# Kernel tuning notes

Hardware: AMD Instinct MI355X
Metric: run time of the kernel (lower is better)

The kernel has to match this reference:

```python
import jax, jax.numpy as jnp
import numpy as np

B, L, H, NH = 4, 2048, 1024, 8
DK = H // NH   # head_k_dim = 128
DV = H // NH   # head_v_dim = 128
CONV_K, FIR_S, FIR_L = 4, 3, 31
CMAX = 0.2
EPS = 1e-5
CHUNK = 32


def _l2norm(x):
    return x * jax.lax.rsqrt(jnp.sum(x * x, -1, keepdims=True) + 1e-6)


def _rms(x, w):
    return x * jax.lax.rsqrt(jnp.mean(x * x, -1, keepdims=True) + EPS) * w


def _causal_conv(x, w):
    # x: [b, l, d], w: [d, K] depthwise causal FIR (ShortConvolution)
    K = w.shape[1]
    l = x.shape[1]
    xp = jnp.pad(x, ((0, 0), (K - 1, 0), (0, 0)))
    return sum(xp[:, i:i + l, :] * w[:, i][None, None, :] for i in range(K))


def _fir(x, w):
    # x: [b, l, h, d], w: [h, d, K] per-head depthwise causal FIR
    K = w.shape[-1]
    l = x.shape[1]
    xp = jnp.pad(x, ((0, 0), (K - 1, 0), (0, 0), (0, 0)))
    return sum(xp[:, i:i + l] * w[:, :, i][None, None] for i in range(K))


def _delta_rule_chunkwise(q, k, v, beta, chunk=CHUNK):
    # q,k: [b,h,L,dk]; v: [b,h,L,dv]; beta: [b,h,L]; L % chunk == 0
    b, h, Ln, dk = q.shape
    dv = v.shape[-1]
    n = Ln // chunk
    q = _l2norm(q)
    k = _l2norm(k)
    v = v * beta[..., None]
    kb = k * beta[..., None]
    rs = lambda t: t.reshape(b, h, n, chunk, t.shape[-1])
    qc, kc, vc, kbc = rs(q), rs(k), rs(v), rs(kb)
    mask_incl = jnp.triu(jnp.ones((chunk, chunk), dtype=bool), 0)
    mask_strict = jnp.triu(jnp.ones((chunk, chunk), dtype=bool), 1)
    # UT / WY transform: sequential Gaussian-elimination over chunk rows
    attn = jnp.where(mask_incl, 0.0, -(kbc @ jnp.swapaxes(kc, -1, -2)))
    for i in range(1, chunk):
        row = attn[..., i, :]                                   # [b,h,n,c]
        upd = jnp.einsum('bhnj,bhnjk->bhnk', row, attn[..., :i])  # [b,h,n,i]
        attn = attn.at[..., i, :i].add(upd)
    attn = attn + jnp.eye(chunk, dtype=attn.dtype)
    u = attn @ vc    # [b,h,n,c,dv]
    w = attn @ kbc   # [b,h,n,c,dk]
    # sequential scan over chunks carrying state S [b,h,dk,dv]
    mv = lambda t: jnp.moveaxis(t, 2, 0)  # [n,b,h,c,d]
    def step(S, xs):
        q_i, k_i, u_i, w_i = xs
        attn_local = jnp.where(mask_strict, 0.0, q_i @ jnp.swapaxes(k_i, -1, -2))
        u_new = u_i - w_i @ S
        o_i = q_i @ S + attn_local @ u_new
        S = S + jnp.swapaxes(k_i, -1, -2) @ u_new
        return S, o_i
    S0 = jnp.zeros((b, h, dk, dv), dtype=q.dtype)
    S, o = jax.lax.scan(step, S0, (mv(qc), mv(kc), mv(u), mv(w)))
    o = jnp.moveaxis(o, 0, 2).reshape(b, h, Ln, dv)
    return o, S


def _forward(hidden_states, Wq, Wk, Wv, Wb, conv_q_w, conv_k_w, conv_v_w,
             fir_short_w, fir_long_w, floor_W, floor_b, fus_W1, fus_b1,
             fus_W2, fus_b2, norm_pf_w, norm_o_w, Wo):
    b, l, _ = hidden_states.shape
    hs = hidden_states
    q_lin = jax.nn.silu(_causal_conv(hs @ Wq, conv_q_w))
    k_lin = jax.nn.silu(_causal_conv(hs @ Wk, conv_k_w))
    v_lin = jax.nn.silu(_causal_conv(hs @ Wv, conv_v_w))
    q = q_lin.reshape(b, l, NH, DK)
    k = k_lin.reshape(b, l, NH, DK)
    v_direct = v_lin.reshape(b, l, NH, DV)
    beta = jax.nn.sigmoid(hs @ Wb)  # [b,l,h]
    delta_out_t, _ = _delta_rule_chunkwise(
        jnp.transpose(q, (0, 2, 1, 3)), jnp.transpose(k, (0, 2, 1, 3)),
        jnp.transpose(v_direct, (0, 2, 1, 3)), jnp.transpose(beta, (0, 2, 1)))
    delta_out = jnp.transpose(delta_out_t, (0, 2, 1, 3))  # [b,l,h,dv]
    local_short = _fir(v_direct, fir_short_w)
    local_long = _fir(v_direct, fir_long_w)
    floor = jax.nn.sigmoid(hs @ floor_W + floor_b) * CMAX  # [b,l,h]
    fus = jax.nn.gelu(hs @ fus_W1 + fus_b1, approximate=False) @ fus_W2 + fus_b2
    fus = fus.reshape(b, l, NH, 4)
    p_value = jax.nn.sigmoid(fus[..., 3]) * (1.0 - floor)  # context share >= floor
    ctx = jax.nn.softmax(fus[..., :3], axis=-1) * (1.0 - p_value)[..., None]
    o = (ctx[..., 0, None] * local_short + ctx[..., 1, None] * local_long
         + ctx[..., 2, None] * delta_out + p_value[..., None] * v_direct)
    o = _rms(o, norm_pf_w)
    o = _rms(o, norm_o_w)
    return o.reshape(b, l, NH * DV) @ Wo


def setup_inputs() -> dict:
    key = jax.random.key(0)
    ks = jax.random.split(key, 16)
    n = lambda k, shape, s=0.02: jax.random.normal(k, shape, jnp.float32) * s
    fus_b2 = jnp.zeros((NH * 4,), jnp.float32).at[3::4].set(4.0)
    return {
        'hidden_states': jax.random.normal(ks[0], (B, L, H), jnp.float32),
        'Wq': n(ks[1], (H, H)), 'Wk': n(ks[2], (H, H)), 'Wv': n(ks[3], (H, H)),
        'Wb': n(ks[4], (H, NH)),
        'conv_q_w': n(ks[5], (H, CONV_K), 0.2),
        'conv_k_w': n(ks[6], (H, CONV_K), 0.2),
        'conv_v_w': n(ks[7], (H, CONV_K), 0.2),
        'fir_short_w': n(ks[8], (NH, DV, FIR_S), 0.2),
        'fir_long_w': n(ks[9], (NH, DV, FIR_L), 0.2),
        'floor_W': n(ks[10], (H, NH)),
        'floor_b': jnp.full((NH,), float(np.log(CMAX / (1 - CMAX))), jnp.float32),
        'fus_W1': n(ks[11], (H, 2 * H)), 'fus_b1': jnp.zeros((2 * H,), jnp.float32),
        'fus_W2': n(ks[12], (2 * H, NH * 4)), 'fus_b2': fus_b2,
        'norm_pf_w': jnp.ones((DV,), jnp.float32),
        'norm_o_w': jnp.ones((DV,), jnp.float32),
        'Wo': n(ks[13], (H, H)),
    }


def reference(hidden_states, Wq, Wk, Wv, Wb, conv_q_w, conv_k_w, conv_v_w,
              fir_short_w, fir_long_w, floor_W, floor_b, fus_W1, fus_b1,
              fus_W2, fus_b2, norm_pf_w, norm_o_w, Wo):
    return _forward(hidden_states, Wq, Wk, Wv, Wb, conv_q_w, conv_k_w, conv_v_w,
                    fir_short_w, fir_long_w, floor_W, floor_b, fus_W1, fus_b1,
                    fus_W2, fus_b2, norm_pf_w, norm_o_w, Wo)
```

## Files before the change

### kernel.cpp

```cpp
#include <hip/hip_runtime.h>
#include <hip/hip_bf16.h>
#include <cstdint>
#include <cstddef>

#define DEVI static __device__ __forceinline__

typedef __attribute__((ext_vector_type(4))) float f32x4;
typedef __attribute__((ext_vector_type(8))) short s16x8;
typedef unsigned short u16;
typedef unsigned int u32;

DEVI float bf2f(u16 u){ u32 x = ((u32)u) << 16; float f; __builtin_memcpy(&f, &x, 4); return f; }
DEVI u16 f2bf(float f){ u32 x; __builtin_memcpy(&x, &f, 4); u32 r = x + 0x7fffu + ((x >> 16) & 1u); return (u16)(r >> 16); }
DEVI float sigm(float x){ return 1.0f / (1.0f + expf(-x)); }
DEVI f32x4 mfma16(s16x8 a, s16x8 b, f32x4 c){ return __builtin_amdgcn_mfma_f32_16x16x32_bf16(a, b, c, 0, 0, 0); }
DEVI s16x8 pack8(float4 a, float4 b){
  s16x8 v;
  v[0]=(short)f2bf(a.x); v[1]=(short)f2bf(a.y); v[2]=(short)f2bf(a.z); v[3]=(short)f2bf(a.w);
  v[4]=(short)f2bf(b.x); v[5]=(short)f2bf(b.y); v[6]=(short)f2bf(b.z); v[7]=(short)f2bf(b.w);
  return v;
}
DEVI u32 pkbf(float lo, float hi){
  u32 d; asm("v_cvt_pk_bf16_f32 %0, %1, %2" : "=v"(d) : "v"(lo), "v"(hi));
  return d;
}
DEVI s16x8 ld_tr(const u16* p){
  short4 a = *(const short4*)p;
  short4 b = *(const short4*)(p + 4);
  s16x8 v; v[0]=a.x; v[1]=a.y; v[2]=a.z; v[3]=a.w; v[4]=b.x; v[5]=b.y; v[6]=b.z; v[7]=b.w;
  return v;
}

#define GLL16(gp, lp) __builtin_amdgcn_global_load_lds( \
    (const __attribute__((address_space(1))) void*)(gp), \
    (__attribute__((address_space(3))) void*)(lp), 16, 0, 0)

__global__ __launch_bounds__(256) void cvt_bf16_k(const float* __restrict__ src, u16* __restrict__ dst, int n4){
  int i = blockIdx.x * 256 + threadIdx.x;
  if (i < n4){
    float4 v = ((const float4*)src)[i];
    ushort4 o; o.x = f2bf(v.x); o.y = f2bf(v.y); o.z = f2bf(v.z); o.w = f2bf(v.w);
    ((ushort4*)dst)[i] = o;
  }
}

__global__ __launch_bounds__(256) void transpose_bf16_k(const float* __restrict__ src, u16* __restrict__ dst, int K, int N){
  __shared__ float tile[32][33];
  const int n0 = blockIdx.x * 32, k0 = blockIdx.y * 32;
  const int t = threadIdx.x, cc = t & 31, rb = t >> 5;
  #pragma unroll
  for (int it = 0; it < 4; ++it){ int rr = rb + it*8; tile[rr][cc] = src[(size_t)(k0+rr)*N + n0 + cc]; }
  __syncthreads();
  #pragma unroll
  for (int it = 0; it < 4; ++it){ int rr = rb + it*8; dst[(size_t)(n0+rr)*K + k0 + cc] = f2bf(tile[cc][rr]); }
}

__global__ __launch_bounds__(64) void w2pack_k(const float* __restrict__ W2, u16* __restrict__ w2p){
  const int kt = blockIdx.x, nt = blockIdx.y;
  const int lane = threadIdx.x, g = lane >> 4, r = lane & 15;
  float v[8];
  #pragma unroll
  for (int i=0;i<8;++i) v[i] = W2[(size_t)(kt*32 + g*8 + i)*32 + nt*16 + r];
  *(s16x8*)(w2p + (((size_t)kt*2 + nt)*64 + lane)*8) = pack8(make_float4(v[0],v[1],v[2],v[3]),
                                                             make_float4(v[4],v[5],v[6],v[7]));
}

__global__ __launch_bounds__(64) void wbpack_k(const float* __restrict__ Wb, const float* __restrict__ Wfl,
                                              u16* __restrict__ wbp){
  const int kt = blockIdx.x;
  const int lane = threadIdx.x, g = lane >> 4, r = lane & 15;
  float v[8];
  #pragma unroll
  for (int i=0;i<8;++i){
    const int k = kt*32 + g*8 + i;
    v[i] = (r < 8) ? Wb[(size_t)k*8 + r] : Wfl[(size_t)k*8 + (r-8)];
  }
  *(s16x8*)(wbp + ((size_t)kt*64 + lane)*8) = pack8(make_float4(v[0],v[1],v[2],v[3]),
                                                    make_float4(v[4],v[5],v[6],v[7]));
}

template<int EPI>
__global__ __launch_bounds__(256, 2) void gemm_bt(
    const u16* __restrict__ A, const u16* __restrict__ Bt, void* __restrict__ Cout,
    const float* __restrict__ bias, int M, int N, int K)
{
  __shared__ __align__(16) u16 As[128*64];
  __shared__ __align__(16) u16 Bs[128*64];
  const int t = threadIdx.x;
  const int lane = t & 63, w = t >> 6;
  const int wr = w >> 1, wc = w & 1;
  const int g = lane >> 4, r16 = lane & 15;
  const int nwg = gridDim.x * gridDim.y;
  const int bid = blockIdx.x + blockIdx.y * gridDim.x;
  const int swz = (bid & 7) * (nwg >> 3) + (bid >> 3);
  const int m0 = (swz / gridDim.x) * 128, n0 = (swz % gridDim.x) * 128;
  f32x4 acc[4][4];
  #pragma unroll
  for (int i=0;i<4;++i){ f32x4 z = {0,0,0,0}; acc[i][0]=z; acc[i][1]=z; acc[i][2]=z; acc[i][3]=z; }
  const int NK = K / 64;
  const int slot_l = w*64 + lane;
  for (int kt = 0; kt < NK; ++kt){
    __syncthreads();
    #pragma unroll
    for (int j=0;j<4;++j){
      const int sl = j*256 + slot_l;
      const int row = sl >> 3, ch = sl & 7;
      const int chs = ch ^ (row & 7);
      GLL16(A  + (size_t)(m0+row)*K + kt*64 + chs*8, As + (size_t)(j*256 + w*64)*8);
      GLL16(Bt + (size_t)(n0+row)*K + kt*64 + chs*8, Bs + (size_t)(j*256 + w*64)*8);
    }
    __syncthreads();
    #pragma unroll
    for (int kh = 0; kh < 2; ++kh){
      s16x8 af[4], bf_[4];
      #pragma unroll
      for (int i=0;i<4;++i){
        const int arow = wr*64 + i*16 + r16;
        af[i]  = *(const s16x8*)(As + (size_t)arow*64 + (((4*kh+g) ^ (arow&7)))*8);
        const int brow = wc*64 + i*16 + r16;
        bf_[i] = *(const s16x8*)(Bs + (size_t)brow*64 + (((4*kh+g) ^ (brow&7)))*8);
      }
      #pragma unroll
      for (int mi=0;mi<4;++mi)
        #pragma unroll
        for (int ni=0;ni<4;++ni)
          acc[mi][ni] = mfma16(af[mi], bf_[ni], acc[mi][ni]);
    }
  }
  #pragma unroll
  for (int mi=0;mi<4;++mi)
    #pragma unroll
    for (int ni=0;ni<4;++ni){
      const int col = n0 + wc*64 + ni*16 + r16;
      #pragma unroll
      for (int i=0;i<4;++i){
        const int row = m0 + wr*64 + mi*16 + g*4 + i;
        float v = acc[mi][ni][i];
        if (EPI == 0){
          ((u16*)Cout)[(size_t)row*N + col] = f2bf(v);
        } else if (EPI == 1){
          float x = v + bias[col];
          x = 0.5f * x * (1.0f + erff(x * 0.70710678118f));
          ((u16*)Cout)[(size_t)row*N + col] = f2bf(x);
        } else if (EPI == 2){
          ((float*)Cout)[(size_t)row*N + col] = v;
        } else {
          ((u16*)Cout)[(size_t)(col >> 10)*8388608 + (size_t)row*1024 + (col & 1023)] = f2bf(v);
        }
      }
    }
}

__global__ __launch_bounds__(64) void beta_floor_k(
    const u16* __restrict__ hsb, const u16* __restrict__ wbp, const float* __restrict__ flb,
    float* __restrict__ beta, float* __restrict__ flo)
{
  const int m0 = blockIdx.x * 16;
  const int lane = threadIdx.x, g = lane >> 4, r = lane & 15;
  f32x4 acc0 = {0,0,0,0}, acc1 = {0,0,0,0};
  #pragma unroll 4
  for (int kt = 0; kt < 32; kt += 2){
    s16x8 a0 = *(const s16x8*)(hsb + (size_t)(m0+r)*1024 + kt*32 + g*8);
    s16x8 b0 = *(const s16x8*)(wbp + ((size_t)kt*64 + lane)*8);
    s16x8 a1 = *(const s16x8*)(hsb + (size_t)(m0+r)*1024 + (kt+1)*32 + g*8);
    s16x8 b1 = *(const s16x8*)(wbp + ((size_t)(kt+1)*64 + lane)*8);
    acc0 = mfma16(a0, b0, acc0);
    acc1 = mfma16(a1, b1, acc1);
  }
  const float fb = (r >= 8) ? flb[r-8] : 0.f;
  #pragma unroll
  for (int i=0;i<4;++i){
    const int row = m0 + g*4 + i;
    const float v = acc0[i] + acc1[i];
    if (r < 8) beta[(size_t)row*8 + r] = sigm(v);
    else       flo [(size_t)row*8 + (r-8)] = 0.2f * sigm(v + fb);
  }
}

__global__ __launch_bounds__(256) void conv_silu_k(
    const u16* __restrict__ qraw, const u16* __restrict__ kraw, const u16* __restrict__ vraw,
    const float* __restrict__ cwq, const float* __restrict__ cwk, const float* __restrict__ cwv,
    u16* __restrict__ vdir, u16* __restrict__ qn, u16* __restrict__ kn)
{
  const int blk = blockIdx.x;
  const int b = blk >> 7, lt = blk & 127;
  const int l0 = lt * 16;
  const int t = threadIdx.x, c0 = t * 4;
  float wq[16], wk[16], wv[16];
  #pragma unroll
  for (int cc=0; cc<4; ++cc){
    float4 a = *(const float4*)(cwq + (size_t)(c0+cc)*4);
    wq[cc*4+0]=a.x; wq[cc*4+1]=a.y; wq[cc*4+2]=a.z; wq[cc*4+3]=a.w;
    float4 bq = *(const float4*)(cwk + (size_t)(c0+cc)*4);
    wk[cc*4+0]=bq.x; wk[cc*4+1]=bq.y; wk[cc*4+2]=bq.z; wk[cc*4+3]=bq.w;
    float4 c = *(const float4*)(cwv + (size_t)(c0+cc)*4);
    wv[cc*4+0]=c.x; wv[cc*4+1]=c.y; wv[cc*4+2]=c.z; wv[cc*4+3]=c.w;
  }
  float hq[3][4], hk[3][4], hv[3][4];
  #pragma unroll
  for (int i=0;i<3;++i){
    const int ls = l0 - 3 + i;
    if (ls >= 0){
      const size_t base = ((size_t)(b << 11) + ls)*1024 + c0;
      union{ ushort4 v; u16 s[4]; } xq, xk, xv;
      xq.v = *(const ushort4*)(qraw + base);
      xk.v = *(const ushort4*)(kraw + base);
      xv.v = *(const ushort4*)(vraw + base);
      #pragma unroll
      for (int cc=0;cc<4;++cc){ hq[i][cc]=bf2f(xq.s[cc]); hk[i][cc]=bf2f(xk.s[cc]); hv[i][cc]=bf2f(xv.s[cc]); }
    } else {
      #pragma unroll
      for (int cc=0;cc<4;++cc){ hq[i][cc]=0.f; hk[i][cc]=0.f; hv[i][cc]=0.f; }
    }
  }
  float cq[4], ck4[4], cv4[4], nq[4], nk[4], nv[4];
  {
    const size_t base = ((size_t)(b << 11) + l0)*1024 + c0;
    union{ ushort4 v; u16 s[4]; } xq, xk, xv;
    xq.v = *(const ushort4*)(qraw + base);
    xk.v = *(const ushort4*)(kraw + base);
    xv.v = *(const ushort4*)(vraw + base);
    #pragma unroll
    for (int cc=0;cc<4;++cc){ cq[cc]=bf2f(xq.s[cc]); ck4[cc]=bf2f(xk.s[cc]); cv4[cc]=bf2f(xv.s[cc]); }
  }
  const int head = c0 >> 7, d0 = c0 & 127;
  for (int rr = 0; rr < 16; ++rr){
    const int l = l0 + rr;
    if (rr < 15){
      const size_t base = ((size_t)(b << 11) + l + 1)*1024 + c0;
      union{ ushort4 v; u16 s[4]; } xq, xk, xv;
      xq.v = *(const ushort4*)(qraw + base);
      xk.v = *(const ushort4*)(kraw + base);
      xv.v = *(const ushort4*)(vraw + base);
      #pragma unroll
      for (int cc=0;cc<4;++cc){ nq[cc]=bf2f(xq.s[cc]); nk[cc]=bf2f(xk.s[cc]); nv[cc]=bf2f(xv.s[cc]); }
    }
    float qa[4], ka[4], va[4];
    #pragma unroll
    for (int cc=0; cc<4; ++cc){
      qa[cc] = hq[0][cc]*wq[cc*4+0] + hq[1][cc]*wq[cc*4+1] + hq[2][cc]*wq[cc*4+2] + cq[cc]*wq[cc*4+3];
      ka[cc] = hk[0][cc]*wk[cc*4+0] + hk[1][cc]*wk[cc*4+1] + hk[2][cc]*wk[cc*4+2] + ck4[cc]*wk[cc*4+3];
      va[cc] = hv[0][cc]*wv[cc*4+0] + hv[1][cc]*wv[cc*4+1] + hv[2][cc]*wv[cc*4+2] + cv4[cc]*wv[cc*4+3];
    }
    #pragma unroll
    for (int cc=0; cc<4; ++cc){
      qa[cc] = qa[cc]*sigm(qa[cc]); ka[cc] = ka[cc]*sigm(ka[cc]); va[cc] = va[cc]*sigm(va[cc]);
    }
    const int grow = (b << 11) + l;
    ushort4 ov; ov.x=f2bf(va[0]); ov.y=f2bf(va[1]); ov.z=f2bf(va[2]); ov.w=f2bf(va[3]);
    *(ushort4*)(vdir + (size_t)grow*1024 + c0) = ov;
    float ssq = 0.f, ssk = 0.f;
    #pragma unroll
    for (int cc=0; cc<4; ++cc){ ssq += qa[cc]*qa[cc]; ssk += ka[cc]*ka[cc]; }
    #pragma unroll
    for (int m=1; m<32; m<<=1){ ssq += __shfl_xor(ssq, m, 64); ssk += __shfl_xor(ssk, m, 64); }
    const float rq = rsqrtf(ssq + 1e-6f), rk = rsqrtf(ssk + 1e-6f);
    const size_t ob = (((size_t)(b*8 + head))*2048 + l)*128 + d0;
    ushort4 oq, ok;
    oq.x=f2bf(qa[0]*rq); oq.y=f2bf(qa[1]*rq); oq.z=f2bf(qa[2]*rq); oq.w=f2bf(qa[3]*rq);
    ok.x=f2bf(ka[0]*rk); ok.y=f2bf(ka[1]*rk); ok.z=f2bf(ka[2]*rk); ok.w=f2bf(ka[3]*rk);
    *(ushort4*)(qn + ob) = oq;
    *(ushort4*)(kn + ob) = ok;
    #pragma unroll
    for (int cc=0; cc<4; ++cc){
      hq[0][cc]=hq[1][cc]; hq[1][cc]=hq[2][cc]; hq[2][cc]=cq[cc];  cq[cc]=nq[cc];
      hk[0][cc]=hk[1][cc]; hk[1][cc]=hk[2][cc]; hk[2][cc]=ck4[cc]; ck4[cc]=nk[cc];
      hv[0][cc]=hv[1][cc]; hv[1][cc]=hv[2][cc]; hv[2][cc]=cv4[cc]; cv4[cc]=nv[cc];
    }
  }
}

__global__ __launch_bounds__(64) void fus2_k(
    const u16* __restrict__ A, const u16* __restrict__ w2p, const float* __restrict__ b2,
    float* __restrict__ out)
{
  const int m0 = blockIdx.x * 16;
  const int lane = threadIdx.x, g = lane >> 4, r = lane & 15;
  f32x4 acc[2][2];
  #pragma unroll
  for (int nt=0;nt<2;++nt){ f32x4 z = {0,0,0,0}; acc[nt][0]=z; acc[nt][1]=z; }
  #pragma unroll 4
  for (int kt = 0; kt < 64; ++kt){
    s16x8 af = *(const s16x8*)(A + (size_t)(m0+r)*2048 + kt*32 + g*8);
    s16x8 b0 = *(const s16x8*)(w2p + (((size_t)kt*2 + 0)*64 + lane)*8);
    s16x8 b1 = *(const s16x8*)(w2p + (((size_t)kt*2 + 1)*64 + lane)*8);
    acc[0][kt&1] = mfma16(af, b0, acc[0][kt&1]);
    acc[1][kt&1] = mfma16(af, b1, acc[1][kt&1]);
  }
  #pragma unroll
  for (int nt=0;nt<2;++nt){
    const float bb = b2[nt*16 + r];
    #pragma unroll
    for (int i=0;i<4;++i)
      out[(size_t)(m0 + g*4 + i)*32 + nt*16 + r] = acc[nt][0][i] + acc[nt][1][i] + bb;
  }
}

__global__ __launch_bounds__(256, 2) void ut_k(
    const u16* __restrict__ qn, const u16* __restrict__ kn,
    const u16* __restrict__ vdir, const float* __restrict__ beta,
    u16* __restrict__ alocp, u16* __restrict__ updk,
    u16* __restrict__ wpk, u16* __restrict__ knpk)
{
  __shared__ __align__(16) char smem[39680];
  u16*  k_s = (u16*)smem;
  float* Tm = (float*)smem;
  float* Gm = (float*)(smem + 8192);
  float* al = (float*)(smem + 12416);
  float* wl = (float*)(smem + 8192);
  u16*  knT = (u16*)(smem + 17024);
  u16*  vbT = (u16*)(smem + 28288);
  float* bet = (float*)(smem + 39552);

  const int blk = blockIdx.x;
  const int ic = blk & 63, bh = blk >> 6;
  const int b = bh >> 3, h = bh & 7;
  const int l0 = ic * 32;
  const int t = threadIdx.x;
  const int lane = t & 63, w = t >> 6;
  const int g = lane >> 4, r = lane & 15;
  const int mt = w >> 1, nt_g = w & 1;

  const size_t gqk = ((size_t)bh*2048 + l0)*128;

  {
    const int row = t >> 3, sseg = t & 7;
    #pragma unroll
    for (int ss=0; ss<2; ++ss){
      const int s = sseg + ss*8;
      int4 kv = *(const int4*)(kn + gqk + (size_t)row*128 + s*8);
      *(int4*)((char*)k_s + row*256 + ((s ^ (row&7))*16)) = kv;
    }
  }
  {
    const int rp = t & 15, cs = t >> 4;
    const int r0 = 2*rp, r1 = 2*rp + 1;
    union { s16x8 v; u16 u[8]; } k0, k1, v0, v1;
    k0.v = *(const s16x8*)(kn + gqk + (size_t)r0*128 + cs*8);
    k1.v = *(const s16x8*)(kn + gqk + (size_t)r1*128 + cs*8);
    v0.v = *(const s16x8*)(vdir + ((size_t)b*2048 + l0 + r0)*1024 + h*128 + cs*8);
    v1.v = *(const s16x8*)(vdir + ((size_t)b*2048 + l0 + r1)*1024 + h*128 + cs*8);
    const float be0 = beta[((size_t)b*2048 + l0 + r0)*8 + h];
    const float be1 = beta[((size_t)b*2048 + l0 + r1)*8 + h];
    if (t < 32) bet[t] = beta[((size_t)b*2048 + l0 + t)*8 + h];
    #pragma unroll
    for (int i=0;i<8;++i){
      const int d = cs*8 + i;
      *(u32*)(knT + (size_t)d*44 + r0) = (u32)k0.u[i] | ((u32)k1.u[i] << 16);
      u32 lo = f2bf(bf2f(v0.u[i]) * be0);
      u32 hi = f2bf(bf2f(v1.u[i]) * be1);
      *(u32*)(vbT + (size_t)d*44 + r0) = lo | (hi << 16);
    }
  }
  __syncthreads();

  {
    f32x4 gacc = {0,0,0,0}, aacc = {0,0,0,0};
    #pragma unroll
    for (int kt=0; kt<4; ++kt){
      s16x8 afk = *(const s16x8*)(kn + gqk + (size_t)(mt*16+r)*128 + kt*32 + g*8);
      s16x8 afq = *(const s16x8*)(qn + gqk + (size_t)(mt*16+r)*128 + kt*32 + g*8);
      const int brow = nt_g*16 + r;
      s16x8 bfrag = *(const s16x8*)((const char*)k_s + brow*256 + (((kt*4+g) ^ (brow&7))*16));
      gacc = mfma16(afk, bfrag, gacc);
      aacc = mfma16(afq, bfrag, aacc);
    }
    #pragma unroll
    for (int i=0;i<4;++i){
      const int rr = mt*16 + g*4 + i, cc = nt_g*16 + r;
      Gm[rr*33 + cc] = gacc[i];
      al[rr*36 + cc] = (cc <= rr) ? aacc[i] : 0.f;
    }
  }
  __syncthreads();

  if (w == 0){
    const int kk = lane & 15, grp = (lane >> 4) & 1, b0 = grp*16;
    float tc[16];
    #pragma unroll
    for (int j=0;j<16;++j)
      tc[j] = (j > kk) ? (-bet[b0+j] * Gm[(b0+j)*33 + b0+kk]) : 0.f;
    #pragma unroll
    for (int i=1;i<16;++i){
      float upd = 0.f;
      #pragma unroll
      for (int j=0;j<i;++j) upd += __shfl(tc[i], (lane & 48) + j, 64) * tc[j];
      if (kk < i) tc[i] += upd;
    }
    if (lane < 32){
      #pragma unroll
      for (int j=0;j<16;++j) Tm[(b0+j)*36 + b0+kk] = tc[j] + ((j == kk) ? 1.f : 0.f);
      if (grp == 1){
        #pragma unroll
        for (int j=0;j<16;++j) Tm[j*36 + 16 + kk] = 0.f;
      }
    }
  } else if (w == 1){
    #pragma unroll
    for (int m2=0; m2<2; ++m2){
      float4 z0 = *(const float4*)(al + (m2*16+r)*36 + g*8);
      float4 z1 = *(const float4*)(al + (m2*16+r)*36 + g*8 + 4);
      *(s16x8*)(alocp + (((size_t)blk*2 + m2)*64 + lane)*8) = pack8(z0, z1);
    }
  } else {
    #pragma unroll
    for (int q2=0; q2<4; ++q2){
      const int mtd = (w-2)*4 + q2;
      s16x8 vv = ld_tr(knT + (size_t)(mtd*16+r)*44 + g*8);
      *(s16x8*)(knpk + (((size_t)blk*8 + mtd)*64 + lane)*8) = vv;
    }
  }
  __syncthreads();

  {
    const int kP = t >> 4, cP = t & 15;
    float p = 0.f;
    #pragma unroll
    for (int m=0;m<16;++m) p += Gm[(16+kP)*33 + m] * Tm[m*36 + cP];
    al[kP*36 + cP] = -bet[16+kP] * p;
  }
  __syncthreads();

  {
    const int rT = t >> 4, cT = t & 15;
    float s = 0.f;
    #pragma unroll
    for (int k=0;k<16;++k) s += Tm[(16+rT)*36 + 16 + k] * al[k*36 + cT];
    Tm[(16+rT)*36 + cT] = s;
  }
  __syncthreads();

  {
    float bb[8];
    #pragma unroll
    for (int i=0;i<8;++i) bb[i] = bet[g*8+i];
    s16x8 tA[2];
    #pragma unroll
    for (int m2=0; m2<2; ++m2){
      float4 x0 = *(const float4*)(Tm + (m2*16+r)*36 + g*8);
      float4 x1 = *(const float4*)(Tm + (m2*16+r)*36 + g*8 + 4);
      tA[m2] = pack8(x0, x1);
    }
    #pragma unroll
    for (int rr2=0; rr2<2; ++rr2){
      const int nt = rr2*4 + w;
      s16x8 bu   = ld_tr(vbT + (size_t)(nt*16+r)*44 + g*8);
      s16x8 braw = ld_tr(knT + (size_t)(nt*16+r)*44 + g*8);
      s16x8 bw;
      #pragma unroll
      for (int i=0;i<8;++i) bw[i] = (short)f2bf(bf2f((u16)braw[i]) * bb[i]);
      f32x4 zz = {0,0,0,0};
      f32x4 du0 = mfma16(tA[0], bu, zz);
      f32x4 du1 = mfma16(tA[1], bu, zz);
      f32x4 dw0 = mfma16(tA[0], bw, zz);
      f32x4 dw1 = mfma16(tA[1], bw, zz);
      *(s16x8*)(updk + (((size_t)blk*8 + nt)*64 + lane)*8) =
          pack8(make_float4(du0[0],du0[1],du0[2],du0[3]),
                make_float4(du1[0],du1[1],du1[2],du1[3]));
      #pragma unroll
      for (int i=0;i<4;++i){
        wl[(      g*4 + i)*68 + (nt&3)*16 + r] = -dw0[i];
        wl[(16 +  g*4 + i)*68 + (nt&3)*16 + r] = -dw1[i];
      }
      __syncthreads();
      {
        const int mtp = w >> 1, ktp = rr2*2 + (w & 1);
        float4 y0 = *(const float4*)(wl + (mtp*16+r)*68 + (ktp&1)*32 + g*8);
        float4 y1 = *(const float4*)(wl + (mtp*16+r)*68 + (ktp&1)*32 + g*8 + 4);
        *(s16x8*)(wpk + ((((size_t)blk*2 + mtp)*4 + ktp)*64 + lane)*8) = pack8(y0, y1);
      }
      __syncthreads();
    }
  }
}

struct SBuf {
  s16x8 uraw;
  s16x8 wf[8];
  s16x8 q0[4], q1[4];
  s16x8 a0, a1;
  s16x8 kf[8];
};

DEVI void scan_load(SBuf& b, const u16* up, const u16* wp, const u16* qp,
                    const u16* ap, const u16* kp, int r, int g){
  b.uraw = *(const s16x8*)(up);
  #pragma unroll
  for (int j=0;j<8;++j) b.wf[j] = *(const s16x8*)(wp + j*512);
  #pragma unroll
  for (int kt=0;kt<4;++kt){
    b.q0[kt] = *(const s16x8*)(qp + r*128 + kt*32 + g*8);
    b.q1[kt] = *(const s16x8*)(qp + (16+r)*128 + kt*32 + g*8);
  }
  b.a0 = *(const s16x8*)(ap);
  b.a1 = *(const s16x8*)(ap + 512);
  #pragma unroll
  for (int j=0;j<8;++j) b.kf[j] = *(const s16x8*)(kp + j*512);
}

DEVI void scan_step(const SBuf& b, f32x4* Sf, u16* dptr,
                    int srcA, int srcB, bool hi, int r, int g){
  u32 pk0[8], pk1[8];
  #pragma unroll
  for (int m=0;m<8;++m){
    pk0[m] = pkbf(Sf[m][0], Sf[m][1]);
    pk1[m] = pkbf(Sf[m][2], Sf[m][3]);
  }
  s16x8 sf[4];
  #pragma unroll
  for (int kt=0;kt<4;++kt){
    u32 eA0 = __shfl(pk0[kt*2],   srcA, 64), oA0 = __shfl(pk0[kt*2+1], srcA, 64);
    u32 eA1 = __shfl(pk1[kt*2],   srcA, 64), oA1 = __shfl(pk1[kt*2+1], srcA, 64);
    u32 eB0 = __shfl(pk0[kt*2],   srcB, 64), oB0 = __shfl(pk0[kt*2+1], srcB, 64);
    u32 eB1 = __shfl(pk1[kt*2],   srcB, 64), oB1 = __shfl(pk1[kt*2+1], srcB, 64);
    union { u32 w[4]; s16x8 v; } uw;
    uw.w[0] = hi ? oA0 : eA0;
    uw.w[1] = hi ? oA1 : eA1;
    uw.w[2] = hi ? oB0 : eB0;
    uw.w[3] = hi ? oB1 : eB1;
    sf[kt] = uw.v;
  }
  f32x4 unA, unB, unA2 = {0,0,0,0}, unB2 = {0,0,0,0};
  #pragma unroll
  for (int i=0;i<4;++i){ unA[i] = bf2f((u16)b.uraw[i]); unB[i] = bf2f((u16)b.uraw[4+i]); }
  unA  = mfma16(b.wf[0], sf[0], unA);
  unA2 = mfma16(b.wf[2], sf[2], unA2);
  unB  = mfma16(b.wf[4], sf[0], unB);
  unB2 = mfma16(b.wf[6], sf[2], unB2);
  unA  = mfma16(b.wf[1], sf[1], unA);
  unA2 = mfma16(b.wf[3], sf[3], unA2);
  unB  = mfma16(b.wf[5], sf[1], unB);
  unB2 = mfma16(b.wf[7], sf[3], unB2);
  f32x4 o0 = {0,0,0,0}, o1 = {0,0,0,0};
  #pragma unroll
  for (int kt=0;kt<4;++kt){
    o0 = mfma16(b.q0[kt], sf[kt], o0);
    o1 = mfma16(b.q1[kt], sf[kt], o1);
  }
  unA = unA + unA2;
  unB = unB + unB2;
  u32 a0p0 = pkbf(unA[0], unA[1]), a0p1 = pkbf(unA[2], unA[3]);
  u32 a1p0 = pkbf(unB[0], unB[1]), a1p1 = pkbf(unB[2], unB[3]);
  u32 w00 = __shfl(a0p0, srcA, 64), w10 = __shfl(a1p0, srcA, 64);
  u32 w01 = __shfl(a0p1, srcA, 64), w11 = __shfl(a1p1, srcA, 64);
  u32 w02 = __shfl(a0p0, srcB, 64), w12 = __shfl(a1p0, srcB, 64);
  u32 w03 = __shfl(a0p1, srcB, 64), w13 = __shfl(a1p1, srcB, 64);
  union { u32 w[4]; s16x8 v; } uu;
  uu.w[0] = hi ? w10 : w00;
  uu.w[1] = hi ? w11 : w01;
  uu.w[2] = hi ? w12 : w02;
  uu.w[3] = hi ? w13 : w03;
  const s16x8 uf = uu.v;
  o0 = mfma16(b.a0, uf, o0);
  o1 = mfma16(b.a1, uf, o1);
  #pragma unroll
  for (int i=0;i<4;++i){
    dptr[(size_t)(g*4+i)*128]    = f2bf(o0[i]);
    dptr[(size_t)(16+g*4+i)*128] = f2bf(o1[i]);
  }
  #pragma unroll
  for (int m=0;m<8;++m) Sf[m] = mfma16(b.kf[m], uf, Sf[m]);
}

__global__ __launch_bounds__(64, 1) void scan_k(
    const u16* __restrict__ qn, const u16* __restrict__ wpk,
    const u16* __restrict__ updk, const u16* __restrict__ alocp,
    const u16* __restrict__ knpk, u16* __restrict__ delta)
{
  const int blk = blockIdx.x;
  const int sl = blk >> 5, bh = blk & 31;
  const int lane = threadIdx.x;
  const int g = lane >> 4, r = lane & 15;
  const int srcA = (g & 1)*32 + r;
  const int srcB = srcA + 16;
  const bool hi = (g >= 2);
  f32x4 Sf[8];
  #pragma unroll
  for (int m=0;m<8;++m){ f32x4 z = {0,0,0,0}; Sf[m] = z; }

  const u16* upB = updk + ((size_t)bh*64*8 + sl)*512 + (size_t)lane*8;
  const u16* wpB = wpk  + (size_t)bh*64*4096 + (size_t)lane*8;
  const u16* qpB = qn   + (size_t)bh*2048*128;
  const u16* apB = alocp + (size_t)bh*64*1024 + (size_t)lane*8;
  const u16* kpB = knpk + (size_t)bh*64*4096 + (size_t)lane*8;
  u16*       dB  = delta + (size_t)bh*2048*128 + sl*16 + r;

  SBuf A, B;
  scan_load(A, upB, wpB, qpB, apB, kpB, r, g);
  for (int ic = 0; ic < 64; ic += 2){
    scan_load(B, upB + (size_t)(ic+1)*4096, wpB + (size_t)(ic+1)*4096,
              qpB + (size_t)(ic+1)*4096, apB + (size_t)(ic+1)*1024,
              kpB + (size_t)(ic+1)*4096, r, g);
    scan_step(A, Sf, dB + (size_t)ic*4096, srcA, srcB, hi, r, g);
    if (ic + 2 < 64)
      scan_load(A, upB + (size_t)(ic+2)*4096, wpB + (size_t)(ic+2)*4096,
                qpB + (size_t)(ic+2)*4096, apB + (size_t)(ic+2)*1024,
                kpB + (size_t)(ic+2)*4096, r, g);
    scan_step(B, Sf, dB + (size_t)(ic+1)*4096, srcA, srcB, hi, r, g);
  }
}

__global__ __launch_bounds__(256) void fuse_k(
    const u16* __restrict__ vdir, const u16* __restrict__ delta,
    const float* __restrict__ fusv, const float* __restrict__ flo,
    const float* __restrict__ fsw, const float* __restrict__ flw,
    const float* __restrict__ wpf, const float* __restrict__ wno,
    u16* __restrict__ ofin)
{
  __shared__ float vt[94][128];
  __shared__ float fl_s[128*31];
  const int blk = blockIdx.x;
  const int lt = blk & 31, h = (blk >> 5) & 7, b = blk >> 8;
  const int l0 = lt * 64;
  const int t = threadIdx.x;
  for (int i = t; i < 128*31; i += 256) fl_s[i] = flw[(size_t)h*128*31 + i];
  for (int s = t; s < 94*16; s += 256){
    const int rr = s >> 4, cc = (s & 15) * 8;
    const int ls = l0 - 30 + rr;
    if (ls >= 0){
      union { s16x8 v; u16 u[8]; } x;
      x.v = *(const s16x8*)(vdir + ((size_t)b*2048 + ls)*1024 + h*128 + cc);
      *(float4*)&vt[rr][cc]   = make_float4(bf2f(x.u[0]),bf2f(x.u[1]),bf2f(x.u[2]),bf2f(x.u[3]));
      *(float4*)&vt[rr][cc+4] = make_float4(bf2f(x.u[4]),bf2f(x.u[5]),bf2f(x.u[6]),bf2f(x.u[7]));
    } else {
      float4 z = {0,0,0,0};
      *(float4*)&vt[rr][cc] = z; *(float4*)&vt[rr][cc+4] = z;
    }
  }
  __syncthreads();
  const int w = t >> 6, lane = t & 63;
  const int d0 = lane * 2;
  const float wp0 = wpf[d0], wp1 = wpf[d0+1];
  const float wn0 = wno[d0], wn1 = wno[d0+1];
  float fs0[3], fs1[3];
  #pragma unroll
  for (int i=0;i<3;++i){
    fs0[i] = fsw[((size_t)h*128 + d0)*3 + i];
    fs1[i] = fsw[((size_t)h*128 + d0 + 1)*3 + i];
  }
  for (int it = 0; it < 16; ++it){
    const int lr = it*4 + w;
    const int l = l0 + lr;
    const float* fr = fusv + ((size_t)b*2048 + l)*32 + h*4;
    const float f0=fr[0], f1=fr[1], f2=fr[2], f3=fr[3];
    const float flv = flo[((size_t)b*2048 + l)*8 + h];
    const float p = sigm(f3) * (1.f - flv);
    const float mx = fmaxf(f0, fmaxf(f1, f2));
    const float e0 = expf(f0-mx), e1 = expf(f1-mx), e2 = expf(f2-mx);
    const float inv = (1.f - p) / (e0 + e1 + e2);
    const float c0 = e0*inv, c1 = e1*inv, c2 = e2*inv;
    float sh0=0, sh1=0, lg0=0, lg1=0;
    #pragma unroll
    for (int i=0;i<31;++i){
      float2 x = *(const float2*)&vt[lr + i][d0];
      lg0 += x.x * fl_s[d0*31 + i];
      lg1 += x.y * fl_s[(d0+1)*31 + i];
    }
    #pragma unroll
    for (int i=0;i<3;++i){
      float2 x = *(const float2*)&vt[lr + 28 + i][d0];
      sh0 += x.x * fs0[i];
      sh1 += x.y * fs1[i];
    }
    const u32 dl2 = *(const u32*)(delta + (((size_t)(b*8 + h))*2048 + l)*128 + d0);
    const float dlx = bf2f((u16)(dl2 & 0xffffu)), dly = bf2f((u16)(dl2 >> 16));
    float2 vc = *(const float2*)&vt[lr + 30][d0];
    float o0 = c0*sh0 + c1*lg0 + c2*dlx + p*vc.x;
    float o1 = c0*sh1 + c1*lg1 + c2*dly + p*vc.y;
    float ss = o0*o0 + o1*o1;
    #pragma unroll
    for (int m=1; m<64; m<<=1) ss += __shfl_xor(ss, m, 64);
    const float r1 = rsqrtf(ss * (1.f/128.f) + 1e-5f);
    const float a0 = o0*r1*wp0, a1 = o1*r1*wp1;
    float s2 = a0*a0 + a1*a1;
    #pragma unroll
    for (int m=1; m<64; m<<=1) s2 += __shfl_xor(s2, m, 64);
    const float r2 = rsqrtf(s2 * (1.f/128.f) + 1e-5f);
    const u32 h0 = f2bf(a0*r2*wn0), h1 = f2bf(a1*r2*wn1);
    *(u32*)(ofin + ((size_t)b*2048 + l)*1024 + h*128 + d0) = h0 | (h1 << 16);
  }
}

constexpr size_t OFF_HSB  = 0;
constexpr size_t OFF_WQT  = 16777216;
constexpr size_t OFF_WKT  = 18874368;
constexpr size_t OFF_WVT  = 20971520;
constexpr size_t OFF_W1T  = 23068672;
constexpr size_t OFF_WOT  = 27262976;
constexpr size_t OFF_QRAW = 29360128;
constexpr size_t OFF_KRAW = 46137344;
constexpr size_t OFF_VRAW = 62914560;
constexpr size_t OFF_FUSV = 79691776;
constexpr size_t OFF_BETA = 80740352;
constexpr size_t OFF_FLO  = 81002496;
constexpr size_t OFF_VDIR = 81264640;
constexpr size_t OFF_W2P  = 98041856;
constexpr size_t OFF_WBP  = 98172928;
constexpr size_t OFF_QN   = 114819072;
constexpr size_t OFF_KN   = 131596288;
constexpr size_t OFF_ALOC = 148373504;
constexpr size_t OFF_UPDK = 152567808;
constexpr size_t OFF_KNPK = 186122240;

extern "C" void kernel_launch(void* const* d_in, const int* in_sizes, int n_in,
                              void* d_out, int out_size, void* d_ws, size_t ws_size,
                              hipStream_t stream)
{
  const float* hs   = (const float*)d_in[0];
  const float* Wq   = (const float*)d_in[1];
  const float* Wk   = (const float*)d_in[2];
  const float* Wv   = (const float*)d_in[3];
  const float* Wb   = (const float*)d_in[4];
  const float* cq   = (const float*)d_in[5];
  const float* ck   = (const float*)d_in[6];
  const float* cv   = (const float*)d_in[7];
  const float* firs = (const float*)d_in[8];
  const float* firl = (const float*)d_in[9];
  const float* flW  = (const float*)d_in[10];
  const float* flb  = (const float*)d_in[11];
  const float* W1   = (const float*)d_in[12];
  const float* b1   = (const float*)d_in[13];
  const float* W2   = (const float*)d_in[14];
  const float* b2   = (const float*)d_in[15];
  const float* npf  = (const float*)d_in[16];
  const float* now  = (const float*)d_in[17];
  const float* Wo   = (const float*)d_in[18];

  char* ws = (char*)d_ws;
  u16*   hsb   = (u16*)(ws + OFF_HSB);
  u16*   wqT   = (u16*)(ws + OFF_WQT);
  u16*   wkT   = (u16*)(ws + OFF_WKT);
  u16*   wvT   = (u16*)(ws + OFF_WVT);
  u16*   w1T   = (u16*)(ws + OFF_W1T);
  u16*   woT   = (u16*)(ws + OFF_WOT);
  u16*   qraw  = (u16*)(ws + OFF_QRAW);
  u16*   kraw  = (u16*)(ws + OFF_KRAW);
  u16*   vraw  = (u16*)(ws + OFF_VRAW);
  u16*   fus1g = (u16*)(ws + OFF_QRAW);
  float* fusv  = (float*)(ws + OFF_FUSV);
  float* beta  = (float*)(ws + OFF_BETA);
  float* flo   = (float*)(ws + OFF_FLO);
  u16*   vdir  = (u16*)(ws + OFF_VDIR);
  u16*   w2p   = (u16*)(ws + OFF_W2P);
  u16*   wbp   = (u16*)(ws + OFF_WBP);
  u16*   qn    = (u16*)(ws + OFF_QN);
  u16*   kn    = (u16*)(ws + OFF_KN);
  u16*   alocp = (u16*)(ws + OFF_ALOC);
  u16*   updk  = (u16*)(ws + OFF_UPDK);
  u16*   wpk   = (u16*)(ws + OFF_VRAW);
  u16*   knpk  = (u16*)(ws + OFF_KNPK);
  u16*   delta = (u16*)(ws + OFF_QRAW);
  u16*   ofin  = (u16*)(ws + OFF_UPDK);

  cvt_bf16_k<<<8192, 256, 0, stream>>>(hs, hsb, 2097152);
  w2pack_k<<<dim3(64,2), 64, 0, stream>>>(W2, w2p);
  wbpack_k<<<32, 64, 0, stream>>>(Wb, flW, wbp);
  transpose_bf16_k<<<dim3(32,32), 256, 0, stream>>>(Wq, wqT, 1024, 1024);
  transpose_bf16_k<<<dim3(32,32), 256, 0, stream>>>(Wk, wkT, 1024, 1024);
  transpose_bf16_k<<<dim3(32,32), 256, 0, stream>>>(Wv, wvT, 1024, 1024);
  transpose_bf16_k<<<dim3(64,32), 256, 0, stream>>>(W1, w1T, 1024, 2048);
  transpose_bf16_k<<<dim3(32,32), 256, 0, stream>>>(Wo, woT, 1024, 1024);
  beta_floor_k<<<512, 64, 0, stream>>>(hsb, wbp, flb, beta, flo);
  gemm_bt<3><<<dim3(24,64), 256, 0, stream>>>(hsb, wqT, qraw, nullptr, 8192, 3072, 1024);
  conv_silu_k<<<512, 256, 0, stream>>>(qraw, kraw, vraw, cq, ck, cv, vdir, qn, kn);
  gemm_bt<1><<<dim3(16,64), 256, 0, stream>>>(hsb, w1T, fus1g, b1, 8192, 2048, 1024);
  fus2_k<<<512, 64, 0, stream>>>(fus1g, w2p, b2, fusv);
  ut_k<<<2048, 256, 0, stream>>>(qn, kn, vdir, beta, alocp, updk, wpk, knpk);
  scan_k<<<256, 64, 0, stream>>>(qn, wpk, updk, alocp, knpk, delta);
  fuse_k<<<1024, 256, 0, stream>>>(vdir, delta, fusv, flo, firs, firl, npf, now, ofin);
  gemm_bt<2><<<dim3(8,64), 256, 0, stream>>>(ofin, woT, d_out, nullptr, 8192, 1024, 1024);
}
```

Measured before the change: 366.1 us.

## Register-tile FIR in fuse kernel and overlap the two RMS-norm reductions

The fuse kernel no longer stages a 94-row fp32 window of vdir in shared memory. Each wave now owns 16 contiguous rows and loads a 46-row sliding window for its two columns straight into registers, then computes the 31-tap long FIR as a register-blocked outer product over a transposed filter table in LDS. The second RMS-norm sum is rewritten algebraically so both wave reductions run in one interleaved shuffle loop. This cuts LDS traffic and a long serial shuffle chain, at the cost of much higher register pressure (about 124 live floats per thread) and possibly uncoalesced 4-byte global loads.

```diff
diff --git a/kernel.cpp b/kernel.cpp
--- a/kernel.cpp
+++ b/kernel.cpp
@@ -607,29 +607,39 @@
     const float* __restrict__ wpf, const float* __restrict__ wno,
     u16* __restrict__ ofin)
 {
-  __shared__ float vt[94][128];
-  __shared__ float fl_s[128*31];
+  __shared__ float fl_t[31][128];
   const int blk = blockIdx.x;
   const int lt = blk & 31, h = (blk >> 5) & 7, b = blk >> 8;
-  const int l0 = lt * 64;
   const int t = threadIdx.x;
-  for (int i = t; i < 128*31; i += 256) fl_s[i] = flw[(size_t)h*128*31 + i];
-  for (int s = t; s < 94*16; s += 256){
-    const int rr = s >> 4, cc = (s & 15) * 8;
-    const int ls = l0 - 30 + rr;
-    if (ls >= 0){
-      union { s16x8 v; u16 u[8]; } x;
-      x.v = *(const s16x8*)(vdir + ((size_t)b*2048 + ls)*1024 + h*128 + cc);
-      *(float4*)&vt[rr][cc]   = make_float4(bf2f(x.u[0]),bf2f(x.u[1]),bf2f(x.u[2]),bf2f(x.u[3]));
-      *(float4*)&vt[rr][cc+4] = make_float4(bf2f(x.u[4]),bf2f(x.u[5]),bf2f(x.u[6]),bf2f(x.u[7]));
-    } else {
-      float4 z = {0,0,0,0};
-      *(float4*)&vt[rr][cc] = z; *(float4*)&vt[rr][cc+4] = z;
-    }
-  }
-  __syncthreads();
   const int w = t >> 6, lane = t & 63;
   const int d0 = lane * 2;
+  const int l0 = lt*64 + w*16;
+  for (int j = t; j < 3968; j += 256){
+    const int d = j / 31, i = j - d*31;
+    fl_t[i][d] = flw[(size_t)h*3968 + j];
+  }
+  __syncthreads();
+  float wlo[46], whi[46];
+  #pragma unroll
+  for (int j = 0; j < 46; ++j){
+    const int ls = l0 - 30 + j;
+    u32 x = 0;
+    if (ls >= 0) x = *(const u32*)(vdir + ((size_t)b*2048 + ls)*1024 + h*128 + d0);
+    wlo[j] = bf2f((u16)(x & 0xffffu));
+    whi[j] = bf2f((u16)(x >> 16));
+  }
+  float lg0[16], lg1[16];
+  #pragma unroll
+  for (int rr = 0; rr < 16; ++rr){ lg0[rr] = 0.f; lg1[rr] = 0.f; }
+  #pragma unroll
+  for (int i = 0; i < 31; ++i){
+    const float2 wv = *(const float2*)&fl_t[i][d0];
+    #pragma unroll
+    for (int rr = 0; rr < 16; ++rr){
+      lg0[rr] += wlo[rr + i] * wv.x;
+      lg1[rr] += whi[rr + i] * wv.y;
+    }
+  }
   const float wp0 = wpf[d0], wp1 = wpf[d0+1];
   const float wn0 = wno[d0], wn1 = wno[d0+1];
   float fs0[3], fs1[3];
@@ -638,9 +648,9 @@
     fs0[i] = fsw[((size_t)h*128 + d0)*3 + i];
     fs1[i] = fsw[((size_t)h*128 + d0 + 1)*3 + i];
   }
-  for (int it = 0; it < 16; ++it){
-    const int lr = it*4 + w;
-    const int l = l0 + lr;
+  #pragma unroll
+  for (int rr = 0; rr < 16; ++rr){
+    const int l = l0 + rr;
     const float* fr = fusv + ((size_t)b*2048 + l)*32 + h*4;
     const float f0=fr[0], f1=fr[1], f2=fr[2], f3=fr[3];
     const float flv = flo[((size_t)b*2048 + l)*8 + h];
@@ -649,34 +659,23 @@
     const float e0 = expf(f0-mx), e1 = expf(f1-mx), e2 = expf(f2-mx);
     const float inv = (1.f - p) / (e0 + e1 + e2);
     const float c0 = e0*inv, c1 = e1*inv, c2 = e2*inv;
-    float sh0=0, sh1=0, lg0=0, lg1=0;
-    #pragma unroll
-    for (int i=0;i<31;++i){
-      float2 x = *(const float2*)&vt[lr + i][d0];
-      lg0 += x.x * fl_s[d0*31 + i];
-      lg1 += x.y * fl_s[(d0+1)*31 + i];
-    }
-    #pragma unroll
-    for (int i=0;i<3;++i){
-      float2 x = *(const float2*)&vt[lr + 28 + i][d0];
-      sh0 += x.x * fs0[i];
-      sh1 += x.y * fs1[i];
-    }
+    const float sh0 = wlo[rr+28]*fs0[0] + wlo[rr+29]*fs0[1] + wlo[rr+30]*fs0[2];
+    const float sh1 = whi[rr+28]*fs1[0] + whi[rr+29]*fs1[1] + whi[rr+30]*fs1[2];
     const u32 dl2 = *(const u32*)(delta + (((size_t)(b*8 + h))*2048 + l)*128 + d0);
     const float dlx = bf2f((u16)(dl2 & 0xffffu)), dly = bf2f((u16)(dl2 >> 16));
-    float2 vc = *(const float2*)&vt[lr + 30][d0];
-    float o0 = c0*sh0 + c1*lg0 + c2*dlx + p*vc.x;
-    float o1 = c0*sh1 + c1*lg1 + c2*dly + p*vc.y;
+    float o0 = c0*sh0 + c1*lg0[rr] + c2*dlx + p*wlo[rr+30];
+    float o1 = c0*sh1 + c1*lg1[rr] + c2*dly + p*whi[rr+30];
+    const float b0 = o0*wp0, b1 = o1*wp1;
     float ss = o0*o0 + o1*o1;
-    #pragma unroll
-    for (int m=1; m<64; m<<=1) ss += __shfl_xor(ss, m, 64);
+    float tt = b0*b0 + b1*b1;
+    #pragma unroll
+    for (int m=1; m<64; m<<=1){
+      ss += __shfl_xor(ss, m, 64);
+      tt += __shfl_xor(tt, m, 64);
+    }
     const float r1 = rsqrtf(ss * (1.f/128.f) + 1e-5f);
-    const float a0 = o0*r1*wp0, a1 = o1*r1*wp1;
-    float s2 = a0*a0 + a1*a1;
-    #pragma unroll
-    for (int m=1; m<64; m<<=1) s2 += __shfl_xor(s2, m, 64);
-    const float r2 = rsqrtf(s2 * (1.f/128.f) + 1e-5f);
-    const u32 h0 = f2bf(a0*r2*wn0), h1 = f2bf(a1*r2*wn1);
+    const float r2 = rsqrtf(r1*r1*tt * (1.f/128.f) + 1e-5f);
+    const u32 h0 = f2bf(o0*r1*wp0*r2*wn0), h1 = f2bf(o1*r1*wp1*r2*wn1);
     *(u32*)(ofin + ((size_t)b*2048 + l)*1024 + h*128 + d0) = h0 | (h1 << 16);
   }
 }
```

Result: faster. 350.2 us (-4.3%).
